# Performance work log

Hardware: AMD Instinct MI355X
Metric: run time of the kernel (lower is better)

## Reference

```python
import jax, jax.numpy as jnp
import numpy as np

LAT = (4, 24, 24, 24, 24, 3, 3)  # [mu, L0, L1, L2, L3, 3, 3]


def setup_inputs() -> dict:
    key = jax.random.key(0)
    k1, k2 = jax.random.split(key)
    U_re = jax.random.normal(k1, LAT, dtype=jnp.float32)
    U_im = jax.random.normal(k2, LAT, dtype=jnp.float32)
    return {"U_re": U_re, "U_im": U_im}


def _polyakov_dir(Umu, axis, L):
    """P(x) = prod_{k=0}^{L-1} U_mu(x + k*mu_hat) via a sequential scan of
    batched 3x3 complex matmuls. Umu: [L0,L1,L2,L3,3,3] complex."""

    def step(carry, _):
        P, Ush = carry
        Ush = jnp.roll(Ush, -1, axis=axis)  # U_mu(x + (k)*mu_hat)
        P = jnp.einsum('...ij,...jk->...ik', P, Ush)
        return (P, Ush), None

    (P, _), _ = jax.lax.scan(step, (Umu, Umu), None, length=L - 1)
    return P


def reference(U_re, U_im):
    U = jax.lax.complex(U_re, U_im)  # complex64 link field
    loops = jnp.stack([
        _polyakov_dir(U[mu], mu, U.shape[1 + mu]) for mu in range(4)
    ])  # [4, L0, L1, L2, L3, 3, 3] complex
    # return real/imag stacked so output is a real array
    return jnp.stack([loops.real, loops.imag])
```

## Files before the change

### kernel.cpp

```cpp
#include <hip/hip_runtime.h>

#define LSIZE 24
#define VOL (LSIZE*LSIZE*LSIZE*LSIZE)
#define NLINES (LSIZE*LSIZE*LSIZE)
#define LPB 8
#define TPB (LPB*LSIZE)
#define NSLOT TPB

__device__ __forceinline__ void copy9(float* d, const float* s) {
#pragma unroll
  for (int e = 0; e < 9; ++e) d[e] = s[e];
}

__device__ __forceinline__ void cmul(const float* ar, const float* ai,
                                     const float* br, const float* bi,
                                     float* or_, float* oi_) {
#pragma unroll
  for (int i = 0; i < 3; ++i) {
#pragma unroll
    for (int j = 0; j < 3; ++j) {
      float sr = 0.f, si = 0.f;
#pragma unroll
      for (int m = 0; m < 3; ++m) {
        float x = ar[i*3+m], y = ai[i*3+m];
        float u = br[m*3+j], v = bi[m*3+j];
        sr = fmaf(x, u, sr);
        sr = fmaf(-y, v, sr);
        si = fmaf(x, v, si);
        si = fmaf(y, u, si);
      }
      or_[i*3+j] = sr;
      oi_[i*3+j] = si;
    }
  }
}

__device__ __forceinline__ void lds_put(float* lds, int slot, const float* re, const float* im) {
#pragma unroll
  for (int e = 0; e < 9; ++e) {
    lds[e * NSLOT + slot]       = re[e];
    lds[(9 + e) * NSLOT + slot] = im[e];
  }
}
__device__ __forceinline__ void lds_get(const float* lds, int slot, float* re, float* im) {
#pragma unroll
  for (int e = 0; e < 9; ++e) {
    re[e] = lds[e * NSLOT + slot];
    im[e] = lds[(9 + e) * NSLOT + slot];
  }
}

__global__ __launch_bounds__(TPB, 4) void polyakov_scan(
    const float* __restrict__ U_re, const float* __restrict__ U_im,
    float* __restrict__ out) {
  __shared__ float lds[18 * NSLOT];

  int gt = threadIdx.x;
  int lineLocal = gt % LPB;
  int k = gt / LPB;
  int slot = gt;

  int L = blockIdx.x * LPB + lineLocal;
  int mu = L / NLINES;
  int l  = L - mu * NLINES;
  int cC = l % LSIZE;
  int cB = (l / LSIZE) % LSIZE;
  int cA = l / (LSIZE*LSIZE);

  int x0, x1, x2, x3, st;
  if (mu == 0)      { x0 = 0;  x1 = cA; x2 = cB; x3 = cC; st = LSIZE*LSIZE*LSIZE; }
  else if (mu == 1) { x0 = cA; x1 = 0;  x2 = cB; x3 = cC; st = LSIZE*LSIZE; }
  else if (mu == 2) { x0 = cA; x1 = cB; x2 = 0;  x3 = cC; st = LSIZE; }
  else              { x0 = cA; x1 = cB; x2 = cC; x3 = 0;  st = 1; }
  int s0 = ((x0*LSIZE + x1)*LSIZE + x2)*LSIZE + x3;
  int site = s0 + k * st;

  const float* inR = U_re + (size_t)mu * (VOL*9) + (size_t)site * 9;
  const float* inI = U_im + (size_t)mu * (VOL*9) + (size_t)site * 9;

  float Ur[9], Ui[9];
#pragma unroll
  for (int e = 0; e < 9; ++e) { Ur[e] = inR[e]; Ui[e] = inI[e]; }

  float Ar[9], Ai[9], Br[9], Bi[9], Tr[9], Ti[9];

  copy9(Ar, Ur); copy9(Ai, Ui);
#pragma unroll
  for (int d = 1; d < LSIZE; d <<= 1) {
    lds_put(lds, slot, Ar, Ai);
    __syncthreads();
    if (k >= d) lds_get(lds, slot - d * LPB, Br, Bi);
    __syncthreads();
    if (k >= d) {
      cmul(Br, Bi, Ar, Ai, Tr, Ti);
      copy9(Ar, Tr); copy9(Ai, Ti);
    }
  }
  lds_put(lds, slot, Ar, Ai);
  __syncthreads();
  float Apr[9], Api[9];
  if (k >= 1) {
    lds_get(lds, slot - LPB, Apr, Api);
  } else {
#pragma unroll
    for (int e = 0; e < 9; ++e) { Apr[e] = (e == 0 || e == 4 || e == 8) ? 1.f : 0.f; Api[e] = 0.f; }
  }
  __syncthreads();

  copy9(Ar, Ur); copy9(Ai, Ui);
#pragma unroll
  for (int d = 1; d < LSIZE; d <<= 1) {
    lds_put(lds, slot, Ar, Ai);
    __syncthreads();
    if (k + d < LSIZE) lds_get(lds, slot + d * LPB, Br, Bi);
    __syncthreads();
    if (k + d < LSIZE) {
      cmul(Ar, Ai, Br, Bi, Tr, Ti);
      copy9(Ar, Tr); copy9(Ai, Ti);
    }
  }

  cmul(Ar, Ai, Apr, Api, Tr, Ti);

  float* outR = out + (size_t)mu * (VOL*9) + (size_t)site * 9;
  float* outI = out + (size_t)(4 + mu) * (VOL*9) + (size_t)site * 9;
#pragma unroll
  for (int e = 0; e < 9; ++e) { outR[e] = Tr[e]; outI[e] = Ti[e]; }
}

extern "C" void kernel_launch(void* const* d_in, const int* in_sizes, int n_in,
                              void* d_out, int out_size, void* d_ws, size_t ws_size,
                              hipStream_t stream) {
  const float* U_re = (const float*)d_in[0];
  const float* U_im = (const float*)d_in[1];
  float* out = (float*)d_out;
  int nblocks = 4 * NLINES / LPB;
  hipLaunchKernelGGL(polyakov_scan, dim3(nblocks), dim3(TPB), 0, stream, U_re, U_im, out);
}
```

Measured before the change: 189.9 us.

## Chunk three links per thread and use wavefront shuffle scans for Polyakov loops

Each thread now loads three consecutive links along the line and multiplies them locally. The cyclic products are then formed with an 8-lane prefix and suffix scan using wavefront shuffles instead of a 24-thread LDS scan with block-wide barriers. The aim is to remove the shared-memory traffic and __syncthreads calls and to cut the number of scan steps. In exchange, register pressure rises with many 3x3 complex temporaries, and each thread performs more matrix multiplies.

```diff
diff --git a/kernel.cpp b/kernel.cpp
--- a/kernel.cpp
+++ b/kernel.cpp
@@ -3,18 +3,14 @@
 #define LSIZE 24
 #define VOL (LSIZE*LSIZE*LSIZE*LSIZE)
 #define NLINES (LSIZE*LSIZE*LSIZE)
-#define LPB 8
-#define TPB (LPB*LSIZE)
-#define NSLOT TPB
+#define CHUNK 3
+#define TPL 8
+#define LPB 32
+#define TPB 256
 
-__device__ __forceinline__ void copy9(float* d, const float* s) {
-#pragma unroll
-  for (int e = 0; e < 9; ++e) d[e] = s[e];
-}
-
-__device__ __forceinline__ void cmul(const float* ar, const float* ai,
-                                     const float* br, const float* bi,
-                                     float* or_, float* oi_) {
+__device__ __forceinline__ void cmul(const float* __restrict__ ar, const float* __restrict__ ai,
+                                     const float* __restrict__ br, const float* __restrict__ bi,
+                                     float* __restrict__ or_, float* __restrict__ oi_) {
 #pragma unroll
   for (int i = 0; i < 3; ++i) {
 #pragma unroll
@@ -35,97 +31,139 @@
   }
 }
 
-__device__ __forceinline__ void lds_put(float* lds, int slot, const float* re, const float* im) {
+__device__ __forceinline__ void cp9(float* dr, float* di, const float* sr, const float* si) {
+#pragma unroll
+  for (int e = 0; e < 9; ++e) { dr[e] = sr[e]; di[e] = si[e]; }
+}
+
+__device__ __forceinline__ void setid(float* r, float* im) {
+#pragma unroll
+  for (int e = 0; e < 9; ++e) { r[e] = (e == 0 || e == 4 || e == 8) ? 1.f : 0.f; im[e] = 0.f; }
+}
+
+__device__ __forceinline__ void shup(float* dr, float* di, const float* sr, const float* si, int delta) {
 #pragma unroll
   for (int e = 0; e < 9; ++e) {
-    lds[e * NSLOT + slot]       = re[e];
-    lds[(9 + e) * NSLOT + slot] = im[e];
+    dr[e] = __shfl_up(sr[e], (unsigned)delta, 64);
+    di[e] = __shfl_up(si[e], (unsigned)delta, 64);
   }
 }
-__device__ __forceinline__ void lds_get(const float* lds, int slot, float* re, float* im) {
+__device__ __forceinline__ void shdn(float* dr, float* di, const float* sr, const float* si, int delta) {
 #pragma unroll
   for (int e = 0; e < 9; ++e) {
-    re[e] = lds[e * NSLOT + slot];
-    im[e] = lds[(9 + e) * NSLOT + slot];
+    dr[e] = __shfl_down(sr[e], (unsigned)delta, 64);
+    di[e] = __shfl_down(si[e], (unsigned)delta, 64);
   }
 }
 
-__global__ __launch_bounds__(TPB, 4) void polyakov_scan(
+__global__ __launch_bounds__(TPB, 2) void polyakov_chunk(
     const float* __restrict__ U_re, const float* __restrict__ U_im,
     float* __restrict__ out) {
-  __shared__ float lds[18 * NSLOT];
+  const int lane = threadIdx.x & 63;
+  const int wv   = threadIdx.x >> 6;
+  const int lineBase = blockIdx.x * LPB + wv * (64 / TPL);
+  const int mu = lineBase / NLINES;
 
-  int gt = threadIdx.x;
-  int lineLocal = gt % LPB;
-  int k = gt / LPB;
-  int slot = gt;
+  int tl, ll, sh;
+  if (mu == 3) { tl = lane & 7; ll = lane >> 3; sh = 1; }
+  else         { tl = lane >> 3; ll = lane & 7; sh = 8; }
 
-  int L = blockIdx.x * LPB + lineLocal;
-  int mu = L / NLINES;
-  int l  = L - mu * NLINES;
-  int cC = l % LSIZE;
-  int cB = (l / LSIZE) % LSIZE;
-  int cA = l / (LSIZE*LSIZE);
+  const int L  = lineBase + ll;
+  const int l  = L - mu * NLINES;
+  const int cC = l % LSIZE;
+  const int cB = (l / LSIZE) % LSIZE;
+  const int cA = l / (LSIZE*LSIZE);
 
   int x0, x1, x2, x3, st;
   if (mu == 0)      { x0 = 0;  x1 = cA; x2 = cB; x3 = cC; st = LSIZE*LSIZE*LSIZE; }
   else if (mu == 1) { x0 = cA; x1 = 0;  x2 = cB; x3 = cC; st = LSIZE*LSIZE; }
   else if (mu == 2) { x0 = cA; x1 = cB; x2 = 0;  x3 = cC; st = LSIZE; }
   else              { x0 = cA; x1 = cB; x2 = cC; x3 = 0;  st = 1; }
-  int s0 = ((x0*LSIZE + x1)*LSIZE + x2)*LSIZE + x3;
-  int site = s0 + k * st;
+  const int s0 = ((x0*LSIZE + x1)*LSIZE + x2)*LSIZE + x3;
+  const int k0 = tl * CHUNK;
 
-  const float* inR = U_re + (size_t)mu * (VOL*9) + (size_t)site * 9;
-  const float* inI = U_im + (size_t)mu * (VOL*9) + (size_t)site * 9;
+  const float* __restrict__ bR = U_re + (size_t)mu * (VOL*9);
+  const float* __restrict__ bI = U_im + (size_t)mu * (VOL*9);
 
-  float Ur[9], Ui[9];
+  float U0r[9], U0i[9], U1r[9], U1i[9], U2r[9], U2i[9];
+  {
+    const float* p = bR + (size_t)(s0 + (k0+0)*st) * 9;
+    const float* q = bI + (size_t)(s0 + (k0+0)*st) * 9;
 #pragma unroll
-  for (int e = 0; e < 9; ++e) { Ur[e] = inR[e]; Ui[e] = inI[e]; }
-
-  float Ar[9], Ai[9], Br[9], Bi[9], Tr[9], Ti[9];
-
-  copy9(Ar, Ur); copy9(Ai, Ui);
+    for (int e = 0; e < 9; ++e) { U0r[e] = p[e]; U0i[e] = q[e]; }
+  }
+  {
+    const float* p = bR + (size_t)(s0 + (k0+1)*st) * 9;
+    const float* q = bI + (size_t)(s0 + (k0+1)*st) * 9;
 #pragma unroll
-  for (int d = 1; d < LSIZE; d <<= 1) {
-    lds_put(lds, slot, Ar, Ai);
-    __syncthreads();
-    if (k >= d) lds_get(lds, slot - d * LPB, Br, Bi);
-    __syncthreads();
-    if (k >= d) {
-      cmul(Br, Bi, Ar, Ai, Tr, Ti);
-      copy9(Ar, Tr); copy9(Ai, Ti);
-    }
+    for (int e = 0; e < 9; ++e) { U1r[e] = p[e]; U1i[e] = q[e]; }
   }
-  lds_put(lds, slot, Ar, Ai);
-  __syncthreads();
-  float Apr[9], Api[9];
-  if (k >= 1) {
-    lds_get(lds, slot - LPB, Apr, Api);
-  } else {
+  {
+    const float* p = bR + (size_t)(s0 + (k0+2)*st) * 9;
+    const float* q = bI + (size_t)(s0 + (k0+2)*st) * 9;
 #pragma unroll
-    for (int e = 0; e < 9; ++e) { Apr[e] = (e == 0 || e == 4 || e == 8) ? 1.f : 0.f; Api[e] = 0.f; }
-  }
-  __syncthreads();
-
-  copy9(Ar, Ur); copy9(Ai, Ui);
-#pragma unroll
-  for (int d = 1; d < LSIZE; d <<= 1) {
-    lds_put(lds, slot, Ar, Ai);
-    __syncthreads();
-    if (k + d < LSIZE) lds_get(lds, slot + d * LPB, Br, Bi);
-    __syncthreads();
-    if (k + d < LSIZE) {
-      cmul(Ar, Ai, Br, Bi, Tr, Ti);
-      copy9(Ar, Tr); copy9(Ai, Ti);
-    }
+    for (int e = 0; e < 9; ++e) { U2r[e] = p[e]; U2i[e] = q[e]; }
   }
 
-  cmul(Ar, Ai, Apr, Api, Tr, Ti);
+  float A1r[9], A1i[9], Br[9], Bi[9], S1r[9], S1i[9];
+  cmul(U0r, U0i, U1r, U1i, A1r, A1i);
+  cmul(A1r, A1i, U2r, U2i, Br,  Bi);
+  cmul(U1r, U1i, U2r, U2i, S1r, S1i);
 
-  float* outR = out + (size_t)mu * (VOL*9) + (size_t)site * 9;
-  float* outI = out + (size_t)(4 + mu) * (VOL*9) + (size_t)site * 9;
+  float Tr[9], Ti[9], Yr[9], Yi[9];
+
+  float Xr[9], Xi[9];
+  cp9(Xr, Xi, Br, Bi);
 #pragma unroll
-  for (int e = 0; e < 9; ++e) { outR[e] = Tr[e]; outI[e] = Ti[e]; }
+  for (int d = 1; d < TPL; d <<= 1) {
+    shup(Yr, Yi, Xr, Xi, d * sh);
+    if (tl >= d) { cmul(Yr, Yi, Xr, Xi, Tr, Ti); cp9(Xr, Xi, Tr, Ti); }
+  }
+
+  float Zr[9], Zi[9];
+  cp9(Zr, Zi, Br, Bi);
+#pragma unroll
+  for (int d = 1; d < TPL; d <<= 1) {
+    shdn(Yr, Yi, Zr, Zi, d * sh);
+    if (tl + d < TPL) { cmul(Zr, Zi, Yr, Yi, Tr, Ti); cp9(Zr, Zi, Tr, Ti); }
+  }
+
+  float Pr[9], Pi[9], Qr[9], Qi[9];
+  shup(Pr, Pi, Xr, Xi, sh);
+  if (tl == 0) setid(Pr, Pi);
+  shdn(Qr, Qi, Zr, Zi, sh);
+  if (tl == TPL - 1) setid(Qr, Qi);
+
+  float Rr[9], Ri[9];
+  cmul(Qr, Qi, Pr, Pi, Rr, Ri);
+
+  float* oR = out + (size_t)mu * (VOL*9);
+  float* oI = out + (size_t)(4 + mu) * (VOL*9);
+  float Wr[9], Wi[9];
+
+  cmul(Br, Bi, Rr, Ri, Tr, Ti);
+  {
+    float* pr = oR + (size_t)(s0 + (k0+0)*st) * 9;
+    float* pi = oI + (size_t)(s0 + (k0+0)*st) * 9;
+#pragma unroll
+    for (int e = 0; e < 9; ++e) { pr[e] = Tr[e]; pi[e] = Ti[e]; }
+  }
+  cmul(Rr, Ri, U0r, U0i, Tr, Ti);
+  cmul(S1r, S1i, Tr, Ti, Wr, Wi);
+  {
+    float* pr = oR + (size_t)(s0 + (k0+1)*st) * 9;
+    float* pi = oI + (size_t)(s0 + (k0+1)*st) * 9;
+#pragma unroll
+    for (int e = 0; e < 9; ++e) { pr[e] = Wr[e]; pi[e] = Wi[e]; }
+  }
+  cmul(Rr, Ri, A1r, A1i, Tr, Ti);
+  cmul(U2r, U2i, Tr, Ti, Wr, Wi);
+  {
+    float* pr = oR + (size_t)(s0 + (k0+2)*st) * 9;
+    float* pi = oI + (size_t)(s0 + (k0+2)*st) * 9;
+#pragma unroll
+    for (int e = 0; e < 9; ++e) { pr[e] = Wr[e]; pi[e] = Wi[e]; }
+  }
 }
 
 extern "C" void kernel_launch(void* const* d_in, const int* in_sizes, int n_in,
@@ -135,5 +173,5 @@
   const float* U_im = (const float*)d_in[1];
   float* out = (float*)d_out;
   int nblocks = 4 * NLINES / LPB;
-  hipLaunchKernelGGL(polyakov_scan, dim3(nblocks), dim3(TPB), 0, stream, U_re, U_im, out);
+  hipLaunchKernelGGL(polyakov_chunk, dim3(nblocks), dim3(TPB), 0, stream, U_re, U_im, out);
 }
```

New measurement: 197.0 us. 1.04x slower.

## Stage lines in LDS and run a register-blocked wave-level scan with bpermute

Applied to the files above, without the earlier changes.

The kernel now stages 16 lines' worth of link matrices into padded LDS with coalesced loads, including a separate layout for the contiguous mu=3 direction. Each thread then owns 3 consecutive links, and prefix and suffix products are scanned across 8 thread groups with ds_bpermute instead of block-wide LDS round trips and barriers. Results are written back through LDS so the global stores are coalesced. The aim is to cut barrier count, LDS traffic and uncoalesced 9-float accesses, at the cost of more complex matmuls per thread and higher register pressure.

```diff
diff --git a/kernel.cpp b/kernel.cpp
--- a/kernel.cpp
+++ b/kernel.cpp
@@ -3,18 +3,14 @@
 #define LSIZE 24
 #define VOL (LSIZE*LSIZE*LSIZE*LSIZE)
 #define NLINES (LSIZE*LSIZE*LSIZE)
-#define LPB 8
-#define TPB (LPB*LSIZE)
-#define NSLOT TPB
-
-__device__ __forceinline__ void copy9(float* d, const float* s) {
-#pragma unroll
-  for (int e = 0; e < 9; ++e) d[e] = s[e];
-}
-
-__device__ __forceinline__ void cmul(const float* ar, const float* ai,
-                                     const float* br, const float* bi,
-                                     float* or_, float* oi_) {
+#define LPB 16
+#define TPB 128
+#define SLABSTRIDE (LPB*9 + 1)
+#define ARRSTRIDE (LSIZE*SLABSTRIDE)
+
+__device__ __forceinline__ void cmul(const float* __restrict__ ar, const float* __restrict__ ai,
+                                     const float* __restrict__ br, const float* __restrict__ bi,
+                                     float* __restrict__ or_, float* __restrict__ oi_) {
 #pragma unroll
   for (int i = 0; i < 3; ++i) {
 #pragma unroll
@@ -35,97 +31,174 @@
   }
 }
 
-__device__ __forceinline__ void lds_put(float* lds, int slot, const float* re, const float* im) {
+__device__ __forceinline__ void cp9(float* dr, float* di, const float* sr, const float* si) {
+#pragma unroll
+  for (int e = 0; e < 9; ++e) { dr[e] = sr[e]; di[e] = si[e]; }
+}
+
+__device__ __forceinline__ void setid(float* r, float* im) {
+#pragma unroll
+  for (int e = 0; e < 9; ++e) { r[e] = (e == 0 || e == 4 || e == 8) ? 1.f : 0.f; im[e] = 0.f; }
+}
+
+__device__ __forceinline__ void ldm9(const float* __restrict__ L, float* v) {
+#pragma unroll
+  for (int e = 0; e < 9; ++e) v[e] = L[e];
+}
+__device__ __forceinline__ void stm9(float* __restrict__ L, const float* v) {
+#pragma unroll
+  for (int e = 0; e < 9; ++e) L[e] = v[e];
+}
+
+__device__ __forceinline__ void bperm9x2(float* dr, float* di,
+                                         const float* sr, const float* si, int srclane) {
+  int a = (srclane & 63) << 2;
 #pragma unroll
   for (int e = 0; e < 9; ++e) {
-    lds[e * NSLOT + slot]       = re[e];
-    lds[(9 + e) * NSLOT + slot] = im[e];
-  }
-}
-__device__ __forceinline__ void lds_get(const float* lds, int slot, float* re, float* im) {
-#pragma unroll
-  for (int e = 0; e < 9; ++e) {
-    re[e] = lds[e * NSLOT + slot];
-    im[e] = lds[(9 + e) * NSLOT + slot];
-  }
-}
-
-__global__ __launch_bounds__(TPB, 4) void polyakov_scan(
+    dr[e] = __int_as_float(__builtin_amdgcn_ds_bpermute(a, __float_as_int(sr[e])));
+    di[e] = __int_as_float(__builtin_amdgcn_ds_bpermute(a, __float_as_int(si[e])));
+  }
+}
+
+__global__ __launch_bounds__(TPB, 2) void polyakov_staged(
     const float* __restrict__ U_re, const float* __restrict__ U_im,
     float* __restrict__ out) {
-  __shared__ float lds[18 * NSLOT];
-
-  int gt = threadIdx.x;
-  int lineLocal = gt % LPB;
-  int k = gt / LPB;
-  int slot = gt;
-
-  int L = blockIdx.x * LPB + lineLocal;
-  int mu = L / NLINES;
-  int l  = L - mu * NLINES;
-  int cC = l % LSIZE;
-  int cB = (l / LSIZE) % LSIZE;
-  int cA = l / (LSIZE*LSIZE);
-
-  int x0, x1, x2, x3, st;
-  if (mu == 0)      { x0 = 0;  x1 = cA; x2 = cB; x3 = cC; st = LSIZE*LSIZE*LSIZE; }
-  else if (mu == 1) { x0 = cA; x1 = 0;  x2 = cB; x3 = cC; st = LSIZE*LSIZE; }
-  else if (mu == 2) { x0 = cA; x1 = cB; x2 = 0;  x3 = cC; st = LSIZE; }
-  else              { x0 = cA; x1 = cB; x2 = cC; x3 = 0;  st = 1; }
-  int s0 = ((x0*LSIZE + x1)*LSIZE + x2)*LSIZE + x3;
-  int site = s0 + k * st;
-
-  const float* inR = U_re + (size_t)mu * (VOL*9) + (size_t)site * 9;
-  const float* inI = U_im + (size_t)mu * (VOL*9) + (size_t)site * 9;
-
-  float Ur[9], Ui[9];
-#pragma unroll
-  for (int e = 0; e < 9; ++e) { Ur[e] = inR[e]; Ui[e] = inI[e]; }
-
-  float Ar[9], Ai[9], Br[9], Bi[9], Tr[9], Ti[9];
-
-  copy9(Ar, Ur); copy9(Ai, Ui);
-#pragma unroll
-  for (int d = 1; d < LSIZE; d <<= 1) {
-    lds_put(lds, slot, Ar, Ai);
-    __syncthreads();
-    if (k >= d) lds_get(lds, slot - d * LPB, Br, Bi);
-    __syncthreads();
-    if (k >= d) {
-      cmul(Br, Bi, Ar, Ai, Tr, Ti);
-      copy9(Ar, Tr); copy9(Ai, Ti);
-    }
-  }
-  lds_put(lds, slot, Ar, Ai);
+  __shared__ float lds[2 * ARRSTRIDE];
+
+  const int t = threadIdx.x;
+  const int lane = t & 63;
+  const int w = t >> 6;
+
+  const int Lb = blockIdx.x * LPB;
+  const int mu = Lb / NLINES;
+  const int l0 = Lb - mu * NLINES;
+
+  int st, e0, e1, e2;
+  if (mu == 0)      { st = 13824; e0 = 576;   e1 = 24;  e2 = 1;  }
+  else if (mu == 1) { st = 576;   e0 = 13824; e1 = 24;  e2 = 1;  }
+  else if (mu == 2) { st = 24;    e0 = 13824; e1 = 576; e2 = 1;  }
+  else              { st = 1;     e0 = 13824; e1 = 576; e2 = 24; }
+
+  const float* __restrict__ gR = U_re + (size_t)mu * (VOL*9);
+  const float* __restrict__ gI = U_im + (size_t)mu * (VOL*9);
+
+  if (mu != 3) {
+#pragma unroll
+    for (int p = 0; p < 6; ++p) {
+      int u = p * TPB + t;
+      int slab = u >> 5;
+      int r = u & 31;
+      int arr = r >> 4;
+      int line = r & 15;
+      int l = l0 + line;
+      int cC = l % LSIZE; int q = l / LSIZE; int cB = q % LSIZE; int cA = q / LSIZE;
+      int site = cA*e0 + cB*e1 + cC*e2 + slab * st;
+      const float* g = (arr ? gI : gR) + (size_t)site * 9;
+      float* L = lds + arr*ARRSTRIDE + slab*SLABSTRIDE + line*9;
+#pragma unroll
+      for (int e = 0; e < 9; ++e) L[e] = g[e];
+    }
+  } else {
+#pragma unroll
+    for (int p = 0; p < 6; ++p) {
+      int u = p * TPB + t;
+      int line = u / 48;
+      int r = u - 48 * line;
+      int arr = r / 24;
+      int k = r - 24 * arr;
+      int site = (l0 + line) * 24 + k;
+      const float* g = (arr ? gI : gR) + (size_t)site * 9;
+      float* L = lds + arr*ARRSTRIDE + k*SLABSTRIDE + line*9;
+#pragma unroll
+      for (int e = 0; e < 9; ++e) L[e] = g[e];
+    }
+  }
   __syncthreads();
-  float Apr[9], Api[9];
-  if (k >= 1) {
-    lds_get(lds, slot - LPB, Apr, Api);
+
+  const int tl = lane >> 3;
+  const int ll = lane & 7;
+  const int line_b = w * 8 + ll;
+  const int k0 = 3 * tl;
+
+  float* mR = lds + line_b * 9;
+  float* mI = lds + ARRSTRIDE + line_b * 9;
+
+  float Xr[9], Xi[9], Zr[9], Zi[9], Yr[9], Yi[9], Tr[9], Ti[9], Rr[9], Ri[9];
+
+  ldm9(mR + (k0+0)*SLABSTRIDE, Xr); ldm9(mI + (k0+0)*SLABSTRIDE, Xi);
+  ldm9(mR + (k0+1)*SLABSTRIDE, Yr); ldm9(mI + (k0+1)*SLABSTRIDE, Yi);
+  cmul(Xr, Xi, Yr, Yi, Tr, Ti);
+  ldm9(mR + (k0+2)*SLABSTRIDE, Yr); ldm9(mI + (k0+2)*SLABSTRIDE, Yi);
+  cmul(Tr, Ti, Yr, Yi, Zr, Zi);
+  cp9(Xr, Xi, Zr, Zi);
+
+#pragma unroll
+  for (int d = 1; d < 8; d <<= 1) {
+    bperm9x2(Yr, Yi, Xr, Xi, lane - 8*d);
+    if (tl >= d) { cmul(Yr, Yi, Xr, Xi, Tr, Ti); cp9(Xr, Xi, Tr, Ti); }
+  }
+#pragma unroll
+  for (int d = 1; d < 8; d <<= 1) {
+    bperm9x2(Yr, Yi, Zr, Zi, lane + 8*d);
+    if (tl + d < 8) { cmul(Zr, Zi, Yr, Yi, Tr, Ti); cp9(Zr, Zi, Tr, Ti); }
+  }
+
+  bperm9x2(Tr, Ti, Zr, Zi, lane + 8);
+  if (tl == 7) setid(Tr, Ti);
+  bperm9x2(Yr, Yi, Xr, Xi, lane - 8);
+  if (tl == 0) setid(Yr, Yi);
+  cmul(Tr, Ti, Yr, Yi, Rr, Ri);
+
+  ldm9(mR + (k0+2)*SLABSTRIDE, Yr); ldm9(mI + (k0+2)*SLABSTRIDE, Yi);
+  cmul(Yr, Yi, Rr, Ri, Tr, Ti);
+  ldm9(mR + (k0+1)*SLABSTRIDE, Xr); ldm9(mI + (k0+1)*SLABSTRIDE, Xi);
+  cmul(Xr, Xi, Tr, Ti, Zr, Zi);
+  ldm9(mR + (k0+0)*SLABSTRIDE, Yr); ldm9(mI + (k0+0)*SLABSTRIDE, Yi);
+
+  cmul(Yr, Yi, Zr, Zi, Rr, Ri);
+  stm9(mR + (k0+0)*SLABSTRIDE, Rr); stm9(mI + (k0+0)*SLABSTRIDE, Ri);
+  cmul(Zr, Zi, Yr, Yi, Rr, Ri);
+  stm9(mR + (k0+1)*SLABSTRIDE, Rr); stm9(mI + (k0+1)*SLABSTRIDE, Ri);
+  cmul(Tr, Ti, Yr, Yi, Zr, Zi);
+  cmul(Zr, Zi, Xr, Xi, Rr, Ri);
+  stm9(mR + (k0+2)*SLABSTRIDE, Rr); stm9(mI + (k0+2)*SLABSTRIDE, Ri);
+
+  __syncthreads();
+
+  float* __restrict__ oRg = out + (size_t)mu * (VOL*9);
+  float* __restrict__ oIg = out + (size_t)(4 + mu) * (VOL*9);
+
+  if (mu != 3) {
+#pragma unroll
+    for (int p = 0; p < 6; ++p) {
+      int u = p * TPB + t;
+      int slab = u >> 5;
+      int r = u & 31;
+      int arr = r >> 4;
+      int line = r & 15;
+      int l = l0 + line;
+      int cC = l % LSIZE; int q = l / LSIZE; int cB = q % LSIZE; int cA = q / LSIZE;
+      int site = cA*e0 + cB*e1 + cC*e2 + slab * st;
+      float* g = (arr ? oIg : oRg) + (size_t)site * 9;
+      const float* L = lds + arr*ARRSTRIDE + slab*SLABSTRIDE + line*9;
+#pragma unroll
+      for (int e = 0; e < 9; ++e) g[e] = L[e];
+    }
   } else {
 #pragma unroll
-    for (int e = 0; e < 9; ++e) { Apr[e] = (e == 0 || e == 4 || e == 8) ? 1.f : 0.f; Api[e] = 0.f; }
-  }
-  __syncthreads();
-
-  copy9(Ar, Ur); copy9(Ai, Ui);
-#pragma unroll
-  for (int d = 1; d < LSIZE; d <<= 1) {
-    lds_put(lds, slot, Ar, Ai);
-    __syncthreads();
-    if (k + d < LSIZE) lds_get(lds, slot + d * LPB, Br, Bi);
-    __syncthreads();
-    if (k + d < LSIZE) {
-      cmul(Ar, Ai, Br, Bi, Tr, Ti);
-      copy9(Ar, Tr); copy9(Ai, Ti);
-    }
-  }
-
-  cmul(Ar, Ai, Apr, Api, Tr, Ti);
-
-  float* outR = out + (size_t)mu * (VOL*9) + (size_t)site * 9;
-  float* outI = out + (size_t)(4 + mu) * (VOL*9) + (size_t)site * 9;
-#pragma unroll
-  for (int e = 0; e < 9; ++e) { outR[e] = Tr[e]; outI[e] = Ti[e]; }
+    for (int p = 0; p < 6; ++p) {
+      int u = p * TPB + t;
+      int line = u / 48;
+      int r = u - 48 * line;
+      int arr = r / 24;
+      int k = r - 24 * arr;
+      int site = (l0 + line) * 24 + k;
+      float* g = (arr ? oIg : oRg) + (size_t)site * 9;
+      const float* L = lds + arr*ARRSTRIDE + k*SLABSTRIDE + line*9;
+#pragma unroll
+      for (int e = 0; e < 9; ++e) g[e] = L[e];
+    }
+  }
 }
 
 extern "C" void kernel_launch(void* const* d_in, const int* in_sizes, int n_in,
@@ -135,5 +208,5 @@
   const float* U_im = (const float*)d_in[1];
   float* out = (float*)d_out;
   int nblocks = 4 * NLINES / LPB;
-  hipLaunchKernelGGL(polyakov_scan, dim3(nblocks), dim3(TPB), 0, stream, U_re, U_im, out);
-}
+  hipLaunchKernelGGL(polyakov_staged, dim3(nblocks), dim3(TPB), 0, stream, U_re, U_im, out);
+}
```

Result: faster. 182.9 us (-3.7%).
